# Kernel tuning notes

Measured on AMD Instinct MI355X. Metric: run time of the kernel, lower is better.

Reference implementation:

```python
import jax, jax.numpy as jnp
import numpy as np

B, T, D, H = 4, 2048, 1024, 16
DH = D // H  # 64


def setup_inputs() -> dict:
    key = jax.random.key(0)
    ks = jax.random.split(key, 6)
    s = 0.02
    x = jax.random.normal(ks[0], (B, T, D), dtype=jnp.float32)
    # causal mask: True (1) marks positions to be masked out
    mask = jnp.triu(jnp.ones((T, T), dtype=bool), k=1)[None, None, :, :]
    WQ = jax.random.normal(ks[1], (D, D), dtype=jnp.float32) * s
    WK = jax.random.normal(ks[2], (D, D), dtype=jnp.float32) * s
    WV = jax.random.normal(ks[3], (D, D), dtype=jnp.float32) * s
    WO = jax.random.normal(ks[4], (D, D), dtype=jnp.float32) * s
    z = jnp.zeros((D,), dtype=jnp.float32)
    return {"x": x, "mask": mask, "WQ": WQ, "bQ": z, "WK": WK, "bK": z,
            "WV": WV, "bV": z, "WO": WO, "bO": z}


def reference(x, mask, WQ, bQ, WK, bK, WV, bV, WO, bO):
    Bc, Tc, Dc = x.shape
    def split_heads(t):  # [B,T,D] -> [B,H,T,DH]
        return t.reshape(Bc, Tc, H, DH).transpose(0, 2, 1, 3)
    q = split_heads(x @ WQ + bQ)
    k = split_heads(x @ WK + bK)
    v = split_heads(x @ WV + bV)
    qk = jnp.einsum("bhqd,bhkd->bhqk", q, k) / jnp.sqrt(jnp.float32(DH))
    qk = qk + mask.astype(qk.dtype) * (-1e9)
    attn = jax.nn.softmax(qk, axis=-1)
    ctx = jnp.einsum("bhqk,bhkd->bhqd", attn, v)  # [B,H,T,DH]
    ctx = ctx.transpose(0, 2, 1, 3).reshape(Bc, Tc, Dc)
    return ctx @ WO + bO
```

## Files before the change

kernel.cpp:

```cpp
#include <hip/hip_runtime.h>
#include <hip/hip_bf16.h>
#include <stdint.h>

#define T_SEQ   2048
#define D_MODEL 1024
#define NHEAD   16
#define DHEAD   64
#define BATCH   4
#define MTOK    (BATCH * T_SEQ)

typedef __attribute__((ext_vector_type(4))) float f32x4;
typedef __attribute__((ext_vector_type(16))) float f32x16;
typedef __attribute__((ext_vector_type(8))) short bf16x8;
typedef __attribute__((ext_vector_type(4))) short s16x4;
typedef __attribute__((ext_vector_type(4))) unsigned u32x4;
typedef __attribute__((ext_vector_type(2))) unsigned u32x2;

__device__ __forceinline__ f32x4 mfma16(bf16x8 a, bf16x8 b, f32x4 c) {
  return __builtin_amdgcn_mfma_f32_16x16x32_bf16(a, b, c, 0, 0, 0);
}
__device__ __forceinline__ f32x16 mfma32(bf16x8 a, bf16x8 b, f32x16 c) {
  return __builtin_amdgcn_mfma_f32_32x32x16_bf16(a, b, c, 0, 0, 0);
}

__device__ __forceinline__ short f2bf(float f) {
  __hip_bfloat16 h = __float2bfloat16(f);
  return *reinterpret_cast<short*>(&h);
}

__device__ __forceinline__ unsigned cvtpk(float a, float b) {
  unsigned r;
  asm("v_cvt_pk_bf16_f32 %0, %1, %2" : "=v"(r) : "v"(a), "v"(b));
  return r;
}

__device__ __forceinline__ u32x2 plswap(unsigned a, unsigned b) {
  return __builtin_amdgcn_permlane32_swap(a, b, false, false);
}

union PB { u32x4 u; bf16x8 b; };

#define GLD_LDS16(gp, lp)                                                      \
  __builtin_amdgcn_global_load_lds(                                            \
      (const __attribute__((address_space(1))) void*)(gp),                     \
      (__attribute__((address_space(3))) void*)(lp), 16, 0, 0)

__global__ __launch_bounds__(256) void transpose_w_kernel(
    const float* __restrict__ W0, const float* __restrict__ W1,
    const float* __restrict__ W2, const float* __restrict__ W3,
    short* __restrict__ out)
{
  const int z = blockIdx.z;
  const float* W = (z == 0) ? W0 : (z == 1) ? W1 : (z == 2) ? W2 : W3;
  short* o = out + (size_t)z * D_MODEL * D_MODEL;
  __shared__ float tile[32][33];
  const int n0 = blockIdx.x * 32, k0 = blockIdx.y * 32;
  const int c = threadIdx.x & 31, r = threadIdx.x >> 5;
#pragma unroll
  for (int i = 0; i < 4; i++)
    tile[r + i * 8][c] = W[(size_t)(k0 + r + i * 8) * D_MODEL + n0 + c];
  __syncthreads();
#pragma unroll
  for (int i = 0; i < 4; i++)
    o[(size_t)(n0 + r + i * 8) * D_MODEL + k0 + c] = f2bf(tile[c][r + i * 8]);
}

__global__ __launch_bounds__(256) void cvt_x_kernel(
    const float* __restrict__ x, short* __restrict__ xb)
{
  const size_t i = (size_t)blockIdx.x * 256 + threadIdx.x;
  const float4 a = ((const float4*)x)[i * 2];
  const float4 b = ((const float4*)x)[i * 2 + 1];
  bf16x8 o;
  o[0] = f2bf(a.x); o[1] = f2bf(a.y); o[2] = f2bf(a.z); o[3] = f2bf(a.w);
  o[4] = f2bf(b.x); o[5] = f2bf(b.y); o[6] = f2bf(b.z); o[7] = f2bf(b.w);
  ((bf16x8*)xb)[i] = o;
}

__global__ __launch_bounds__(256) void gemm_bt(
    const short* __restrict__ A, const short* __restrict__ Bt,
    const float* __restrict__ bias, float* __restrict__ Cp)
{
  __shared__ __align__(16) short As[128 * 32];
  __shared__ __align__(16) short Bs[128 * 32];
  const int tid = threadIdx.x, lane = tid & 63, wid = tid >> 6;
  const int wr = wid >> 1, wc = wid & 1;
  const int lg = lane >> 4, ln = lane & 15;
  const int m0 = blockIdx.x * 128, n0 = blockIdx.y * 128;
  const int lrow = lane >> 2, lchunk = lane & 3;

  f32x4 acc[4][4];
#pragma unroll
  for (int i = 0; i < 4; i++)
#pragma unroll
    for (int j = 0; j < 4; j++) acc[i][j] = {0.f, 0.f, 0.f, 0.f};

  for (int k0 = 0; k0 < 1024; k0 += 32) {
#pragma unroll
    for (int s = 0; s < 2; ++s) {
      const int rbase = (wid * 2 + s) * 16;
      const short* gpa = A + (size_t)(m0 + rbase + lrow) * 1024 + k0 + lchunk * 8;
      GLD_LDS16(gpa, As + rbase * 32);
      const short* gpb = Bt + (size_t)(n0 + rbase + lrow) * 1024 + k0 + lchunk * 8;
      GLD_LDS16(gpb, Bs + rbase * 32);
    }
    __syncthreads();
    bf16x8 a[4], b[4];
#pragma unroll
    for (int mi = 0; mi < 4; mi++)
      a[mi] = *(const bf16x8*)(As + (wr * 64 + mi * 16 + ln) * 32 + lg * 8);
#pragma unroll
    for (int ni = 0; ni < 4; ni++)
      b[ni] = *(const bf16x8*)(Bs + (wc * 64 + ni * 16 + ln) * 32 + lg * 8);
#pragma unroll
    for (int mi = 0; mi < 4; mi++)
#pragma unroll
      for (int ni = 0; ni < 4; ni++)
        acc[mi][ni] = mfma16(a[mi], b[ni], acc[mi][ni]);
    __syncthreads();
  }

#pragma unroll
  for (int mi = 0; mi < 4; mi++)
#pragma unroll
    for (int ni = 0; ni < 4; ni++)
#pragma unroll
      for (int r = 0; r < 4; r++) {
        const int row = m0 + wr * 64 + mi * 16 + lg * 4 + r;
        const int col = n0 + wc * 64 + ni * 16 + ln;
        Cp[(size_t)row * 1024 + col] = acc[mi][ni][r] + bias[col];
      }
}

__global__ __launch_bounds__(256) void gemm_qkv(
    const short* __restrict__ A, const short* __restrict__ Wt,
    const float* __restrict__ bQ, const float* __restrict__ bK,
    const float* __restrict__ bV,
    short* __restrict__ Qb, short* __restrict__ Kb, short* __restrict__ Vt,
    float qscale)
{
  __shared__ __align__(16) short As[128 * 32];
  __shared__ __align__(16) short Bs[128 * 32];
  const int tid = threadIdx.x, lane = tid & 63, wid = tid >> 6;
  const int wr = wid >> 1, wc = wid & 1;
  const int lg = lane >> 4, ln = lane & 15;
  const int m0 = blockIdx.x * 128;
  const int nglob = blockIdx.y * 128;
  const int seg = blockIdx.y >> 3;
  const int n0 = nglob & 1023;
  const short* Bt = Wt + (size_t)nglob * 1024;
  const float* bias = (seg == 0) ? bQ : (seg == 1) ? bK : bV;
  const float scale = (seg == 0) ? qscale : 1.0f;
  const int lrow = lane >> 2, lchunk = lane & 3;

  f32x4 acc[4][4];
#pragma unroll
  for (int i = 0; i < 4; i++)
#pragma unroll
    for (int j = 0; j < 4; j++) acc[i][j] = {0.f, 0.f, 0.f, 0.f};

  for (int k0 = 0; k0 < 1024; k0 += 32) {
#pragma unroll
    for (int s = 0; s < 2; ++s) {
      const int rbase = (wid * 2 + s) * 16;
      const short* gpa = A + (size_t)(m0 + rbase + lrow) * 1024 + k0 + lchunk * 8;
      GLD_LDS16(gpa, As + rbase * 32);
      const short* gpb = Bt + (size_t)(rbase + lrow) * 1024 + k0 + lchunk * 8;
      GLD_LDS16(gpb, Bs + rbase * 32);
    }
    __syncthreads();
    bf16x8 a[4], b[4];
#pragma unroll
    for (int mi = 0; mi < 4; mi++)
      a[mi] = *(const bf16x8*)(As + (wr * 64 + mi * 16 + ln) * 32 + lg * 8);
#pragma unroll
    for (int ni = 0; ni < 4; ni++)
      b[ni] = *(const bf16x8*)(Bs + (wc * 64 + ni * 16 + ln) * 32 + lg * 8);
#pragma unroll
    for (int mi = 0; mi < 4; mi++)
#pragma unroll
      for (int ni = 0; ni < 4; ni++)
        acc[mi][ni] = mfma16(a[mi], b[ni], acc[mi][ni]);
    __syncthreads();
  }

  if (seg == 2) {
    const int bb = m0 >> 11;
    const int tbase = (m0 & 2047) + wr * 64 + lg * 4;
#pragma unroll
    for (int mi = 0; mi < 4; mi++)
#pragma unroll
      for (int ni = 0; ni < 4; ni++) {
        const int col = n0 + wc * 64 + ni * 16 + ln;
        const int hh = col >> 6, dh = col & 63;
        s16x4 w;
#pragma unroll
        for (int r = 0; r < 4; r++) w[r] = f2bf(acc[mi][ni][r] + bias[col]);
        *(s16x4*)(Vt + (size_t)((bb * 16 + hh) * 64 + dh) * T_SEQ +
                  tbase + mi * 16) = w;
      }
  } else {
    short* Cp = (seg == 0) ? Qb : Kb;
#pragma unroll
    for (int mi = 0; mi < 4; mi++)
#pragma unroll
      for (int ni = 0; ni < 4; ni++)
#pragma unroll
        for (int r = 0; r < 4; r++) {
          const int row = m0 + wr * 64 + mi * 16 + lg * 4 + r;
          const int col = n0 + wc * 64 + ni * 16 + ln;
          const float v = (acc[mi][ni][r] + bias[col]) * scale;
          Cp[(size_t)row * 1024 + col] = f2bf(v);
        }
  }
}

__device__ __forceinline__ void tile_chain(
    const bf16x8* kf0, const bf16x8* kf1,
    const bf16x8* vf0, const bf16x8* vf1,
    const bf16x8* qf, const f32x16& zv,
    f32x16& o0, f32x16& o1, float& m_run, float& l_run,
    const int kv0, const int qw, const int q, const int hi)
{
  f32x16 s0, s1;
  __builtin_amdgcn_s_setprio(1);
  s0 = mfma32(kf0[0], qf[0], zv);
#pragma unroll
  for (int c = 1; c < 4; c++) s0 = mfma32(kf0[c], qf[c], s0);
  s1 = mfma32(kf1[0], qf[0], zv);
#pragma unroll
  for (int c = 1; c < 4; c++) s1 = mfma32(kf1[c], qf[c], s1);
  __builtin_amdgcn_s_setprio(0);

  if (kv0 + 63 > qw) {
    const int qrel = q - kv0 - 4 * hi;
#pragma unroll
    for (int r = 0; r < 16; r++) {
      const int cst = (r & 3) + 8 * (r >> 2);
      if (cst > qrel) s0[r] = -3.0e38f;
      if (cst + 32 > qrel) s1[r] = -3.0e38f;
    }
  }

  float mx;
  {
    float t[8];
#pragma unroll
    for (int i = 0; i < 8; i++)
      t[i] = fmaxf(fmaxf(s0[i], s0[i + 8]), fmaxf(s1[i], s1[i + 8]));
    const float a0 = fmaxf(fmaxf(t[0], t[1]), fmaxf(t[2], t[3]));
    const float a1 = fmaxf(fmaxf(t[4], t[5]), fmaxf(t[6], t[7]));
    mx = fmaxf(a0, a1);
    u32x2 r = plswap(__float_as_uint(mx), __float_as_uint(mx));
    mx = fmaxf(__uint_as_float(r[0]), __uint_as_float(r[1]));
  }
  if (!__all(mx - m_run <= 8.0f)) {
    const float mn = fmaxf(m_run, mx);
    const float rr = exp2f(m_run - mn);
    m_run = mn;
    l_run *= rr;
#pragma unroll
    for (int i = 0; i < 16; i++) { o0[i] *= rr; o1[i] *= rr; }
  }
  const float mn = m_run;
#pragma unroll
  for (int i = 0; i < 16; i++) s0[i] = exp2f(s0[i] - mn);
#pragma unroll
  for (int i = 0; i < 16; i++) s1[i] = exp2f(s1[i] - mn);
  float ts;
  {
    float t[8];
#pragma unroll
    for (int i = 0; i < 8; i++) t[i] = (s0[i] + s0[i + 8]) + (s1[i] + s1[i + 8]);
    ts = ((t[0] + t[1]) + (t[2] + t[3])) + ((t[4] + t[5]) + (t[6] + t[7]));
    u32x2 r = plswap(__float_as_uint(ts), __float_as_uint(ts));
    ts = __uint_as_float(r[0]) + __uint_as_float(r[1]);
  }
  l_run += ts;

  PB pb[4];
  {
    unsigned c0 = cvtpk(s0[0], s0[1]),   c1 = cvtpk(s0[2], s0[3]);
    unsigned c2 = cvtpk(s0[4], s0[5]),   c3 = cvtpk(s0[6], s0[7]);
    unsigned c4 = cvtpk(s0[8], s0[9]),   c5 = cvtpk(s0[10], s0[11]);
    unsigned c6 = cvtpk(s0[12], s0[13]), c7 = cvtpk(s0[14], s0[15]);
    u32x2 r02 = plswap(c0, c2), r13 = plswap(c1, c3);
    u32x2 r46 = plswap(c4, c6), r57 = plswap(c5, c7);
    pb[0].u = (u32x4){r02[0], r13[0], r02[1], r13[1]};
    pb[1].u = (u32x4){r46[0], r57[0], r46[1], r57[1]};
  }
  {
    unsigned c0 = cvtpk(s1[0], s1[1]),   c1 = cvtpk(s1[2], s1[3]);
    unsigned c2 = cvtpk(s1[4], s1[5]),   c3 = cvtpk(s1[6], s1[7]);
    unsigned c4 = cvtpk(s1[8], s1[9]),   c5 = cvtpk(s1[10], s1[11]);
    unsigned c6 = cvtpk(s1[12], s1[13]), c7 = cvtpk(s1[14], s1[15]);
    u32x2 r02 = plswap(c0, c2), r13 = plswap(c1, c3);
    u32x2 r46 = plswap(c4, c6), r57 = plswap(c5, c7);
    pb[2].u = (u32x4){r02[0], r13[0], r02[1], r13[1]};
    pb[3].u = (u32x4){r46[0], r57[0], r46[1], r57[1]};
  }

  __builtin_amdgcn_s_setprio(1);
#pragma unroll
  for (int kc = 0; kc < 4; kc++) {
    o0 = mfma32(vf0[kc], pb[kc].b, o0);
    o1 = mfma32(vf1[kc], pb[kc].b, o1);
  }
  __builtin_amdgcn_s_setprio(0);
}

__device__ __forceinline__ void attn_epilogue(
    short* cp, const f32x16& o0, const f32x16& o1, float l_run, int hi)
{
  const float inv = 1.0f / l_run;
#pragma unroll
  for (int g = 0; g < 4; g++) {
    s16x4 w0, w1;
#pragma unroll
    for (int j = 0; j < 4; j++) {
      w0[j] = f2bf(o0[g * 4 + j] * inv);
      w1[j] = f2bf(o1[g * 4 + j] * inv);
    }
    *(s16x4*)(cp + g * 8 + 4 * hi) = w0;
    *(s16x4*)(cp + 32 + g * 8 + 4 * hi) = w1;
  }
}

__global__ __launch_bounds__(256, 2) void attn_fwd(
    const short* __restrict__ Q, const short* __restrict__ K,
    const short* __restrict__ Vt, short* __restrict__ ctx)
{
  const int tid = threadIdx.x, lane = tid & 63, wid = tid >> 6;
  const int hi = lane >> 5, lq = lane & 31;
  const int id = (int)blockIdx.x;
  const int bh = (id & 7) * 8 + ((id >> 3) & 7);
  const int p = (id >> 6) * 4 + wid;
  const int b = bh >> 4, h = bh & 15;

  const int qtA = p, qtB = 63 - p;
  const int qwA = qtA * 32, qwB = qtB * 32;
  const int qA = qwA + lq, qB = qwB + lq;

  bf16x8 qfA[4], qfB[4];
  {
    const short* qpA = Q + (size_t)(b * T_SEQ + qA) * 1024 + h * 64 + hi * 8;
    const short* qpB = Q + (size_t)(b * T_SEQ + qB) * 1024 + h * 64 + hi * 8;
#pragma unroll
    for (int c = 0; c < 4; c++) {
      qfA[c] = *(const bf16x8*)(qpA + c * 16);
      qfB[c] = *(const bf16x8*)(qpB + c * 16);
    }
  }

  f32x16 zv;
#pragma unroll
  for (int i = 0; i < 16; i++) zv[i] = 0.f;

  f32x16 oA0 = zv, oA1 = zv, oB0 = zv, oB1 = zv;
  float mA = -3.0e38f, lA = 0.f, mB = -3.0e38f, lB = 0.f;

  const int ntA = (qwA + 95) >> 6, ntB = (qwB + 95) >> 6;

#pragma unroll 1
  for (int it = 0; it < ntB; ++it) {
    const int kv0 = it * 64;
    bf16x8 kf0[4], kf1[4], vf0[4], vf1[4];
    {
      const short* kp = K + (size_t)(b * T_SEQ + kv0 + lq) * 1024 + h * 64 + hi * 8;
      const short* vp = Vt + (size_t)(bh * 64 + lq) * T_SEQ + kv0 + hi * 8;
#pragma unroll
      for (int c = 0; c < 4; c++) {
        kf0[c] = *(const bf16x8*)(kp + c * 16);
        kf1[c] = *(const bf16x8*)(kp + 32 * 1024 + c * 16);
        vf0[c] = *(const bf16x8*)(vp + c * 16);
        vf1[c] = *(const bf16x8*)(vp + 32 * T_SEQ + c * 16);
      }
    }
    tile_chain(kf0, kf1, vf0, vf1, qfB, zv, oB0, oB1, mB, lB, kv0, qwB, qB, hi);
    if (it < ntA)
      tile_chain(kf0, kf1, vf0, vf1, qfA, zv, oA0, oA1, mA, lA, kv0, qwA, qA, hi);
  }

  attn_epilogue(ctx + (size_t)(b * T_SEQ + qA) * 1024 + h * 64, oA0, oA1, lA, hi);
  attn_epilogue(ctx + (size_t)(b * T_SEQ + qB) * 1024 + h * 64, oB0, oB1, lB, hi);
}

extern "C" void kernel_launch(void* const* d_in, const int* in_sizes, int n_in,
                              void* d_out, int out_size, void* d_ws, size_t ws_size,
                              hipStream_t stream)
{
  (void)in_sizes; (void)n_in; (void)out_size; (void)ws_size;
  const float* x  = (const float*)d_in[0];
  const float* WQ = (const float*)d_in[2];
  const float* bQ = (const float*)d_in[3];
  const float* WK = (const float*)d_in[4];
  const float* bK = (const float*)d_in[5];
  const float* WV = (const float*)d_in[6];
  const float* bV = (const float*)d_in[7];
  const float* WO = (const float*)d_in[8];
  const float* bO = (const float*)d_in[9];
  float* out = (float*)d_out;

  const size_t MB = 1024ull * 1024ull;
  char* w = (char*)d_ws;
  short* xb = (short*)(w);
  short* Wt = (short*)(w + 16 * MB);
  short* Qb = (short*)(w + 24 * MB);
  short* Kb = (short*)(w + 40 * MB);
  short* Vt = (short*)(w + 72 * MB);
  short* ctx = xb;

  transpose_w_kernel<<<dim3(32, 32, 4), 256, 0, stream>>>(WQ, WK, WV, WO, Wt);
  cvt_x_kernel<<<dim3(MTOK * D_MODEL / 8 / 256), 256, 0, stream>>>(x, xb);

  const float qscale = 0.125f * 1.4426950408889634f;
  gemm_qkv<<<dim3(64, 24), 256, 0, stream>>>(xb, Wt, bQ, bK, bV, Qb, Kb, Vt, qscale);

  attn_fwd<<<dim3(512), 256, 0, stream>>>(Qb, Kb, Vt, ctx);

  gemm_bt<<<dim3(64, 8), 256, 0, stream>>>(ctx, Wt + 3ull * D_MODEL * D_MODEL, bO, out);
}
```

Measured before the change: 212.6 us.

## Give each attention wave one query tile and balance causal work across waves

```diff
diff --git a/kernel.cpp b/kernel.cpp
--- a/kernel.cpp
+++ b/kernel.cpp
@@ -326,7 +326,7 @@
   }
 }
 
-__global__ __launch_bounds__(256, 2) void attn_fwd(
+__global__ __launch_bounds__(256, 4) void attn_fwd(
     const short* __restrict__ Q, const short* __restrict__ K,
     const short* __restrict__ Vt, short* __restrict__ ctx)
 {
@@ -334,35 +334,33 @@
   const int hi = lane >> 5, lq = lane & 31;
   const int id = (int)blockIdx.x;
   const int bh = (id & 7) * 8 + ((id >> 3) & 7);
-  const int p = (id >> 6) * 4 + wid;
+  const int s = id >> 6;
   const int b = bh >> 4, h = bh & 15;
 
-  const int qtA = p, qtB = 63 - p;
-  const int qwA = qtA * 32, qwB = qtB * 32;
-  const int qA = qwA + lq, qB = qwB + lq;
-
-  bf16x8 qfA[4], qfB[4];
+  const int cls = (wid + (s >> 2)) & 3;
+  const int qt = (cls == 0) ? s : (cls == 1) ? (31 - s)
+               : (cls == 2) ? (32 + s) : (63 - s);
+  const int qw = qt * 32;
+  const int q = qw + lq;
+
+  bf16x8 qf[4];
   {
-    const short* qpA = Q + (size_t)(b * T_SEQ + qA) * 1024 + h * 64 + hi * 8;
-    const short* qpB = Q + (size_t)(b * T_SEQ + qB) * 1024 + h * 64 + hi * 8;
-#pragma unroll
-    for (int c = 0; c < 4; c++) {
-      qfA[c] = *(const bf16x8*)(qpA + c * 16);
-      qfB[c] = *(const bf16x8*)(qpB + c * 16);
-    }
+    const short* qp = Q + (size_t)(b * T_SEQ + q) * 1024 + h * 64 + hi * 8;
+#pragma unroll
+    for (int c = 0; c < 4; c++) qf[c] = *(const bf16x8*)(qp + c * 16);
   }
 
   f32x16 zv;
 #pragma unroll
   for (int i = 0; i < 16; i++) zv[i] = 0.f;
 
-  f32x16 oA0 = zv, oA1 = zv, oB0 = zv, oB1 = zv;
-  float mA = -3.0e38f, lA = 0.f, mB = -3.0e38f, lB = 0.f;
-
-  const int ntA = (qwA + 95) >> 6, ntB = (qwB + 95) >> 6;
+  f32x16 o0 = zv, o1 = zv;
+  float m_run = -3.0e38f, l_run = 0.f;
+
+  const int nt = (qw + 95) >> 6;
 
 #pragma unroll 1
-  for (int it = 0; it < ntB; ++it) {
+  for (int it = 0; it < nt; ++it) {
     const int kv0 = it * 64;
     bf16x8 kf0[4], kf1[4], vf0[4], vf1[4];
     {
@@ -376,13 +374,10 @@
         vf1[c] = *(const bf16x8*)(vp + 32 * T_SEQ + c * 16);
       }
     }
-    tile_chain(kf0, kf1, vf0, vf1, qfB, zv, oB0, oB1, mB, lB, kv0, qwB, qB, hi);
-    if (it < ntA)
-      tile_chain(kf0, kf1, vf0, vf1, qfA, zv, oA0, oA1, mA, lA, kv0, qwA, qA, hi);
-  }
-
-  attn_epilogue(ctx + (size_t)(b * T_SEQ + qA) * 1024 + h * 64, oA0, oA1, lA, hi);
-  attn_epilogue(ctx + (size_t)(b * T_SEQ + qB) * 1024 + h * 64, oB0, oB1, lB, hi);
+    tile_chain(kf0, kf1, vf0, vf1, qf, zv, o0, o1, m_run, l_run, kv0, qw, q, hi);
+  }
+
+  attn_epilogue(ctx + (size_t)(b * T_SEQ + q) * 1024 + h * 64, o0, o1, l_run, hi);
 }
 
 extern "C" void kernel_launch(void* const* d_in, const int* in_sizes, int n_in,
@@ -416,7 +411,7 @@
   const float qscale = 0.125f * 1.4426950408889634f;
   gemm_qkv<<<dim3(64, 24), 256, 0, stream>>>(xb, Wt, bQ, bK, bV, Qb, Kb, Vt, qscale);
 
-  attn_fwd<<<dim3(512), 256, 0, stream>>>(Qb, Kb, Vt, ctx);
+  attn_fwd<<<dim3(1024), 256, 0, stream>>>(Qb, Kb, Vt, ctx);
 
   gemm_bt<<<dim3(64, 8), 256, 0, stream>>>(ctx, Wt + 3ull * D_MODEL * D_MODEL, bO, out);
 }
```

After: 302.0 us. +42.1%, slower.
